# Optimization experiments

Hardware: AMD Instinct MI355X
Metric: run time of the kernel (lower is better)

## Reference

```python
import jax, jax.numpy as jnp
import numpy as np

B, N, C, H = 8, 1024, 512, 8
DH = C // H
SCALE = DH ** -0.5
NEG = -1.0e9


def setup_inputs() -> dict:
    key = jax.random.key(0)
    ks = jax.random.split(key, 8)
    s = lambda fan: 1.0 / np.sqrt(fan)
    return {
        "x": jax.random.normal(ks[0], (B, N, C), jnp.float32),
        "mask": jnp.ones((B, N), jnp.float32),
        "qkv_w": jax.random.normal(ks[1], (3 * C, C), jnp.float32) * s(C),
        "qkv_b": jnp.zeros((3 * C,), jnp.float32),
        "proj_w_mat": jax.random.normal(ks[2], (C, C), jnp.float32) * s(C),
        "proj_b": jnp.zeros((C,), jnp.float32),
        "pl_w": jax.random.normal(ks[3], (H, H), jnp.float32) * s(H),
        "pl_b": jnp.zeros((H,), jnp.float32),
        "pw_w": jax.random.normal(ks[4], (H, H), jnp.float32) * s(H),
        "pw_b": jnp.zeros((H,), jnp.float32),
    }


def reference(x, mask, qkv_w, qkv_b, proj_w_mat, proj_b, pl_w, pl_b, pw_w, pw_b):
    b, n, c = x.shape
    h = pl_w.shape[0]
    dh = c // h
    # qkv: [B,N,3C] -> [3,B,H,N,Dh]
    qkv = (x @ qkv_w.T + qkv_b).reshape(b, n, 3, h, dh).transpose(2, 0, 3, 1, 4)
    q, k, v = qkv[0] * SCALE, qkv[1], qkv[2]
    # raw scores [B,H,N,N]
    attn = jnp.einsum("bhnd,bhmd->bhnm", q, k)
    # talking-heads pre-softmax mixing (Linear over head dim)
    attn = jnp.einsum("bhnm,gh->bgnm", attn, pl_w) + pl_b[None, :, None, None]
    # mask: [B,N] -> broadcast over heads and query dim (keys masked)
    attn = attn + (1.0 - mask)[:, None, None, :] * NEG
    attn = jax.nn.softmax(attn, axis=-1)
    # talking-heads post-softmax mixing
    attn = jnp.einsum("bhnm,gh->bgnm", attn, pw_w) + pw_b[None, :, None, None]
    out = jnp.einsum("bhnm,bhmd->bhnd", attn, v)
    out = out.transpose(0, 2, 1, 3).reshape(b, n, c)
    out = out @ proj_w_mat.T + proj_b
    return (out, attn)
```

## Files before the change

kernel.cpp:

```cpp
#include <hip/hip_runtime.h>
#include <cstddef>

#define B_ 8
#define N_ 1024
#define C_ 512
#define H_ 8
#define DH_ 64
#define QKVLD 1536
#define SCALE_ 0.125f
#define NEG_ -1.0e9f

typedef _Float16 f16;
typedef f16  f16x4 __attribute__((ext_vector_type(4)));
typedef f16  f16x8 __attribute__((ext_vector_type(8)));
typedef float f32x4 __attribute__((ext_vector_type(4)));

static __device__ __forceinline__ f16x4 cvt4(float4 v) {
    f16x4 r; r[0] = (f16)v.x; r[1] = (f16)v.y; r[2] = (f16)v.z; r[3] = (f16)v.w;
    return r;
}

template<int BN, bool BHALF>
__device__ __forceinline__ void gemm_core(
    const float* __restrict__ A, int lda,
    const void* __restrict__ Bv, int ldb,
    const float* __restrict__ bias, float scale,
    float* __restrict__ Cc, int ldc, int K, int bm, int bn)
{
    constexpr int FJ = BN / 32;
    __shared__ __align__(16) f16 Af[128][40];
    __shared__ __align__(16) f16 Bf[BN][40];
    const int tid  = threadIdx.x;
    const int wid  = tid >> 6, lane = tid & 63;
    const int wm   = (wid >> 1) * 64, wn = (wid & 1) * (BN / 2);
    const int lrow = lane & 15, kg = lane >> 4;
    const int ar = tid >> 3, ac = (tid & 7) << 2;
    const int hr = tid >> 2, hc = (tid & 3) << 3;

    f32x4 acc[4][FJ];
#pragma unroll
    for (int i = 0; i < 4; ++i)
#pragma unroll
        for (int j = 0; j < FJ; ++j) acc[i][j] = (f32x4){0.f, 0.f, 0.f, 0.f};

    for (int k0 = 0; k0 < K; k0 += 32) {
        float4 a0 = *(const float4*)(A + (size_t)(bm + ar     ) * lda + k0 + ac);
        float4 a1 = *(const float4*)(A + (size_t)(bm + ar + 32) * lda + k0 + ac);
        float4 a2 = *(const float4*)(A + (size_t)(bm + ar + 64) * lda + k0 + ac);
        float4 a3 = *(const float4*)(A + (size_t)(bm + ar + 96) * lda + k0 + ac);
        float4 b0, b1, b2, b3;
        f16x8  bh;
        if constexpr (!BHALF) {
            const float* Bp = (const float*)Bv;
            b0 = *(const float4*)(Bp + (size_t)(bn + ar     ) * ldb + k0 + ac);
            b1 = *(const float4*)(Bp + (size_t)(bn + ar + 32) * ldb + k0 + ac);
            if constexpr (BN == 128) {
                b2 = *(const float4*)(Bp + (size_t)(bn + ar + 64) * ldb + k0 + ac);
                b3 = *(const float4*)(Bp + (size_t)(bn + ar + 96) * ldb + k0 + ac);
            }
        } else {
            const f16* Bp = (const f16*)Bv;
            bh = *(const f16x8*)(Bp + (size_t)(bn + hr) * ldb + k0 + hc);
        }
        __syncthreads();
        *(f16x4*)&Af[ar     ][ac] = cvt4(a0);
        *(f16x4*)&Af[ar + 32][ac] = cvt4(a1);
        *(f16x4*)&Af[ar + 64][ac] = cvt4(a2);
        *(f16x4*)&Af[ar + 96][ac] = cvt4(a3);
        if constexpr (!BHALF) {
            *(f16x4*)&Bf[ar     ][ac] = cvt4(b0);
            *(f16x4*)&Bf[ar + 32][ac] = cvt4(b1);
            if constexpr (BN == 128) {
                *(f16x4*)&Bf[ar + 64][ac] = cvt4(b2);
                *(f16x4*)&Bf[ar + 96][ac] = cvt4(b3);
            }
        } else {
            *(f16x8*)&Bf[hr][hc] = bh;
        }
        __syncthreads();
        f16x8 af[4], bf[FJ];
#pragma unroll
        for (int i = 0; i < 4; ++i)
            af[i] = *(const f16x8*)&Af[wm + i * 16 + lrow][kg * 8];
#pragma unroll
        for (int j = 0; j < FJ; ++j)
            bf[j] = *(const f16x8*)&Bf[wn + j * 16 + lrow][kg * 8];
#pragma unroll
        for (int i = 0; i < 4; ++i)
#pragma unroll
            for (int j = 0; j < FJ; ++j)
                acc[i][j] = __builtin_amdgcn_mfma_f32_16x16x32_f16(af[i], bf[j], acc[i][j], 0, 0, 0);
    }
#pragma unroll
    for (int j = 0; j < FJ; ++j) {
        const int col = bn + wn + j * 16 + lrow;
        const float bv = bias ? bias[col] : 0.f;
#pragma unroll
        for (int i = 0; i < 4; ++i) {
            const int row0 = bm + wm + i * 16 + kg * 4;
#pragma unroll
            for (int r = 0; r < 4; ++r)
                Cc[(size_t)(row0 + r) * ldc + col] = acc[i][j][r] * scale + bv;
        }
    }
}

__global__ __launch_bounds__(256) void k_qkv(const float* __restrict__ x,
                                             const float* __restrict__ w,
                                             const float* __restrict__ b,
                                             float* __restrict__ o) {
    gemm_core<128, false>(x, C_, w, C_, b, 1.f, o, QKVLD, C_,
                          blockIdx.y * 128, blockIdx.x * 128);
}

__global__ __launch_bounds__(256) void k_proj(const float* __restrict__ o1,
                                              const float* __restrict__ w,
                                              const float* __restrict__ b,
                                              float* __restrict__ o) {
    gemm_core<128, false>(o1, C_, w, C_, b, 1.f, o, C_, C_,
                          blockIdx.y * 128, blockIdx.x * 128);
}

__global__ __launch_bounds__(256) void k_scores(const float* __restrict__ qkv,
                                                float* __restrict__ attn) {
    const int z = blockIdx.z, b = z >> 3, h = z & 7;
    const float* Q  = qkv + (size_t)b * N_ * QKVLD + h * DH_;
    const float* Kp = Q + C_;
    gemm_core<128, false>(Q, QKVLD, Kp, QKVLD, nullptr, SCALE_,
                          attn + (size_t)z * N_ * N_, N_, DH_,
                          blockIdx.y * 128, blockIdx.x * 128);
}

__global__ __launch_bounds__(256) void k_pv(const float* __restrict__ attn,
                                            const f16* __restrict__ vt,
                                            float* __restrict__ out1) {
    const int z = blockIdx.z, b = z >> 3, h = z & 7;
    gemm_core<64, true>(attn + (size_t)z * N_ * N_, N_,
                        vt + (size_t)z * DH_ * N_, N_, nullptr, 1.f,
                        out1 + (size_t)b * N_ * C_ + h * DH_, C_, N_,
                        blockIdx.y * 128, 0);
}

__global__ __launch_bounds__(256) void pack_vt(const float* __restrict__ qkv,
                                               f16* __restrict__ vt) {
    const int z = blockIdx.x, b = z >> 3, h = z & 7;
    const float* V = qkv + (size_t)b * N_ * QKVLD + 2 * C_ + h * DH_;
    f16* O = vt + (size_t)z * DH_ * N_;
    __shared__ __align__(16) f16 T[64][72];
    const int t = threadIdx.x;
    for (int m0 = 0; m0 < N_; m0 += 64) {
#pragma unroll
        for (int it = 0; it < 4; ++it) {
            const int m = (t >> 4) + it * 16, dg = t & 15, d = dg * 4;
            float4 v = *(const float4*)(V + (size_t)(m0 + m) * QKVLD + d);
            T[d + 0][m] = (f16)v.x; T[d + 1][m] = (f16)v.y;
            T[d + 2][m] = (f16)v.z; T[d + 3][m] = (f16)v.w;
        }
        __syncthreads();
#pragma unroll
        for (int it = 0; it < 2; ++it) {
            const int d = (t >> 3) + it * 32, m = (t & 7) << 3;
            *(f16x8*)(O + (size_t)d * N_ + m0 + m) = *(const f16x8*)&T[d][m];
        }
        __syncthreads();
    }
}

__global__ __launch_bounds__(256) void mix_softmax_kernel(
    float* __restrict__ attn, const float* __restrict__ mask,
    const float* __restrict__ pl_w, const float* __restrict__ pl_b,
    const float* __restrict__ pw_w, const float* __restrict__ pw_b)
{
    const int n = blockIdx.x;
    const int b = blockIdx.y;
    const int tid = threadIdx.x;
    __shared__ float w1[64], w2[64], b1[8], b2[8];
    __shared__ float red[4][8];
    if (tid < 64) w1[tid] = pl_w[tid];
    else if (tid < 128) w2[tid - 64] = pw_w[tid - 64];
    else if (tid < 136) b1[tid - 128] = pl_b[tid - 128];
    else if (tid < 144) b2[tid - 136] = pw_b[tid - 136];
    __syncthreads();

    const int m0 = tid << 2;
    const size_t rowbase = ((size_t)(b * H_) * N_ + n) * N_ + m0;
    const size_t hstride = (size_t)N_ * N_;

    float s[8][4];
#pragma unroll
    for (int h = 0; h < 8; ++h) {
        float4 v = *(const float4*)(attn + rowbase + (size_t)h * hstride);
        s[h][0] = v.x; s[h][1] = v.y; s[h][2] = v.z; s[h][3] = v.w;
    }
    float4 mv = *(const float4*)(mask + b * N_ + m0);
    const float mk[4] = {(1.f - mv.x) * NEG_, (1.f - mv.y) * NEG_,
                         (1.f - mv.z) * NEG_, (1.f - mv.w) * NEG_};
    float a[8][4];
#pragma unroll
    for (int g = 0; g < 8; ++g)
#pragma unroll
        for (int j = 0; j < 4; ++j) a[g][j] = b1[g] + mk[j];
#pragma unroll
    for (int h = 0; h < 8; ++h)
#pragma unroll
        for (int g = 0; g < 8; ++g) {
            const float w = w1[g * 8 + h];
#pragma unroll
            for (int j = 0; j < 4; ++j) a[g][j] = fmaf(w, s[h][j], a[g][j]);
        }
    float mx[8];
#pragma unroll
    for (int g = 0; g < 8; ++g)
        mx[g] = fmaxf(fmaxf(a[g][0], a[g][1]), fmaxf(a[g][2], a[g][3]));
#pragma unroll
    for (int g = 0; g < 8; ++g)
        for (int off = 32; off; off >>= 1)
            mx[g] = fmaxf(mx[g], __shfl_xor(mx[g], off));
    const int wv = tid >> 6, ln = tid & 63;
    if (ln == 0) {
#pragma unroll
        for (int g = 0; g < 8; ++g) red[wv][g] = mx[g];
    }
    __syncthreads();
#pragma unroll
    for (int g = 0; g < 8; ++g)
        mx[g] = fmaxf(fmaxf(red[0][g], red[1][g]), fmaxf(red[2][g], red[3][g]));
    __syncthreads();
    float sm[8];
#pragma unroll
    for (int g = 0; g < 8; ++g) {
        float t = 0.f;
#pragma unroll
        for (int j = 0; j < 4; ++j) {
            a[g][j] = __expf(a[g][j] - mx[g]);
            t += a[g][j];
        }
        sm[g] = t;
    }
#pragma unroll
    for (int g = 0; g < 8; ++g)
        for (int off = 32; off; off >>= 1)
            sm[g] += __shfl_xor(sm[g], off);
    if (ln == 0) {
#pragma unroll
        for (int g = 0; g < 8; ++g) red[wv][g] = sm[g];
    }
    __syncthreads();
#pragma unroll
    for (int g = 0; g < 8; ++g) {
        const float inv = 1.f / (red[0][g] + red[1][g] + red[2][g] + red[3][g]);
#pragma unroll
        for (int j = 0; j < 4; ++j) a[g][j] *= inv;
    }
#pragma unroll
    for (int g = 0; g < 8; ++g) {
        float o[4] = {b2[g], b2[g], b2[g], b2[g]};
#pragma unroll
        for (int h = 0; h < 8; ++h) {
            const float w = w2[g * 8 + h];
#pragma unroll
            for (int j = 0; j < 4; ++j) o[j] = fmaf(w, a[h][j], o[j]);
        }
        *(float4*)(attn + rowbase + (size_t)g * hstride) = make_float4(o[0], o[1], o[2], o[3]);
    }
}

extern "C" void kernel_launch(void* const* d_in, const int* in_sizes, int n_in,
                              void* d_out, int out_size, void* d_ws, size_t ws_size,
                              hipStream_t stream)
{
    const float* x      = (const float*)d_in[0];
    const float* mask   = (const float*)d_in[1];
    const float* qkv_w  = (const float*)d_in[2];
    const float* qkv_b  = (const float*)d_in[3];
    const float* proj_w = (const float*)d_in[4];
    const float* proj_b = (const float*)d_in[5];
    const float* pl_w   = (const float*)d_in[6];
    const float* pl_b   = (const float*)d_in[7];
    const float* pw_w   = (const float*)d_in[8];
    const float* pw_b   = (const float*)d_in[9];

    float* out  = (float*)d_out;
    float* attn = out + (size_t)B_ * N_ * C_;
    float* qkv  = (float*)d_ws;
    float* out1 = qkv + (size_t)B_ * N_ * 3 * C_;
    f16*   vt   = (f16*)(out1 + (size_t)B_ * N_ * C_);
    (void)in_sizes; (void)n_in; (void)out_size; (void)ws_size;

    k_qkv<<<dim3(QKVLD / 128, B_ * N_ / 128), 256, 0, stream>>>(x, qkv_w, qkv_b, qkv);

    pack_vt<<<dim3(B_ * H_), 256, 0, stream>>>(qkv, vt);

    k_scores<<<dim3(N_ / 128, N_ / 128, B_ * H_), 256, 0, stream>>>(qkv, attn);

    mix_softmax_kernel<<<dim3(N_, B_), 256, 0, stream>>>(attn, mask, pl_w, pl_b, pw_w, pw_b);

    k_pv<<<dim3(1, N_ / 128, B_ * H_), 256, 0, stream>>>(attn, vt, out1);

    k_proj<<<dim3(C_ / 128, B_ * N_ / 128), 256, 0, stream>>>(out1, proj_w, proj_b, out);
}
```

Baseline: 318.2 us.

## Fuse scores, talking-heads softmax, PV and projection into one flash-style kernel

Replaces the separate score GEMM, mix/softmax pass, PV GEMM and projection GEMM with one kernel per 32-query tile. It runs two passes over the keys: the first recomputes scores with online max/sum statistics, the second recomputes them to write the normalized mixed attention, accumulate PV, and then apply the output projection. K and proj_w are pre-packed to fp16. This removes the fp32 attention round-trip read/write between kernels but doubles the QK compute. The grid is also small (256 blocks) with per-lane global K loads, which may limit occupancy and bandwidth.

```diff
diff --git a/kernel.cpp b/kernel.cpp
--- a/kernel.cpp
+++ b/kernel.cpp
@@ -35,7 +35,6 @@
     const int wm   = (wid >> 1) * 64, wn = (wid & 1) * (BN / 2);
     const int lrow = lane & 15, kg = lane >> 4;
     const int ar = tid >> 3, ac = (tid & 7) << 2;
-    const int hr = tid >> 2, hc = (tid & 3) << 3;
 
     f32x4 acc[4][FJ];
 #pragma unroll
@@ -48,48 +47,33 @@
         float4 a1 = *(const float4*)(A + (size_t)(bm + ar + 32) * lda + k0 + ac);
         float4 a2 = *(const float4*)(A + (size_t)(bm + ar + 64) * lda + k0 + ac);
         float4 a3 = *(const float4*)(A + (size_t)(bm + ar + 96) * lda + k0 + ac);
-        float4 b0, b1, b2, b3;
-        f16x8  bh;
-        if constexpr (!BHALF) {
-            const float* Bp = (const float*)Bv;
-            b0 = *(const float4*)(Bp + (size_t)(bn + ar     ) * ldb + k0 + ac);
-            b1 = *(const float4*)(Bp + (size_t)(bn + ar + 32) * ldb + k0 + ac);
-            if constexpr (BN == 128) {
-                b2 = *(const float4*)(Bp + (size_t)(bn + ar + 64) * ldb + k0 + ac);
-                b3 = *(const float4*)(Bp + (size_t)(bn + ar + 96) * ldb + k0 + ac);
-            }
-        } else {
-            const f16* Bp = (const f16*)Bv;
-            bh = *(const f16x8*)(Bp + (size_t)(bn + hr) * ldb + k0 + hc);
-        }
+        const float* Bp = (const float*)Bv;
+        float4 b0 = *(const float4*)(Bp + (size_t)(bn + ar     ) * ldb + k0 + ac);
+        float4 b1 = *(const float4*)(Bp + (size_t)(bn + ar + 32) * ldb + k0 + ac);
+        float4 b2 = *(const float4*)(Bp + (size_t)(bn + ar + 64) * ldb + k0 + ac);
+        float4 b3 = *(const float4*)(Bp + (size_t)(bn + ar + 96) * ldb + k0 + ac);
         __syncthreads();
         *(f16x4*)&Af[ar     ][ac] = cvt4(a0);
         *(f16x4*)&Af[ar + 32][ac] = cvt4(a1);
         *(f16x4*)&Af[ar + 64][ac] = cvt4(a2);
         *(f16x4*)&Af[ar + 96][ac] = cvt4(a3);
-        if constexpr (!BHALF) {
-            *(f16x4*)&Bf[ar     ][ac] = cvt4(b0);
-            *(f16x4*)&Bf[ar + 32][ac] = cvt4(b1);
-            if constexpr (BN == 128) {
-                *(f16x4*)&Bf[ar + 64][ac] = cvt4(b2);
-                *(f16x4*)&Bf[ar + 96][ac] = cvt4(b3);
-            }
-        } else {
-            *(f16x8*)&Bf[hr][hc] = bh;
-        }
-        __syncthreads();
-        f16x8 af[4], bf[FJ];
+        *(f16x4*)&Bf[ar     ][ac] = cvt4(b0);
+        *(f16x4*)&Bf[ar + 32][ac] = cvt4(b1);
+        *(f16x4*)&Bf[ar + 64][ac] = cvt4(b2);
+        *(f16x4*)&Bf[ar + 96][ac] = cvt4(b3);
+        __syncthreads();
+        f16x8 af[4], bfv[FJ];
 #pragma unroll
         for (int i = 0; i < 4; ++i)
             af[i] = *(const f16x8*)&Af[wm + i * 16 + lrow][kg * 8];
 #pragma unroll
         for (int j = 0; j < FJ; ++j)
-            bf[j] = *(const f16x8*)&Bf[wn + j * 16 + lrow][kg * 8];
+            bfv[j] = *(const f16x8*)&Bf[wn + j * 16 + lrow][kg * 8];
 #pragma unroll
         for (int i = 0; i < 4; ++i)
 #pragma unroll
             for (int j = 0; j < FJ; ++j)
-                acc[i][j] = __builtin_amdgcn_mfma_f32_16x16x32_f16(af[i], bf[j], acc[i][j], 0, 0, 0);
+                acc[i][j] = __builtin_amdgcn_mfma_f32_16x16x32_f16(af[i], bfv[j], acc[i][j], 0, 0, 0);
     }
 #pragma unroll
     for (int j = 0; j < FJ; ++j) {
@@ -113,32 +97,30 @@
                           blockIdx.y * 128, blockIdx.x * 128);
 }
 
-__global__ __launch_bounds__(256) void k_proj(const float* __restrict__ o1,
-                                              const float* __restrict__ w,
-                                              const float* __restrict__ b,
-                                              float* __restrict__ o) {
-    gemm_core<128, false>(o1, C_, w, C_, b, 1.f, o, C_, C_,
-                          blockIdx.y * 128, blockIdx.x * 128);
-}
-
-__global__ __launch_bounds__(256) void k_scores(const float* __restrict__ qkv,
-                                                float* __restrict__ attn) {
-    const int z = blockIdx.z, b = z >> 3, h = z & 7;
-    const float* Q  = qkv + (size_t)b * N_ * QKVLD + h * DH_;
-    const float* Kp = Q + C_;
-    gemm_core<128, false>(Q, QKVLD, Kp, QKVLD, nullptr, SCALE_,
-                          attn + (size_t)z * N_ * N_, N_, DH_,
-                          blockIdx.y * 128, blockIdx.x * 128);
-}
-
-__global__ __launch_bounds__(256) void k_pv(const float* __restrict__ attn,
-                                            const f16* __restrict__ vt,
-                                            float* __restrict__ out1) {
-    const int z = blockIdx.z, b = z >> 3, h = z & 7;
-    gemm_core<64, true>(attn + (size_t)z * N_ * N_, N_,
-                        vt + (size_t)z * DH_ * N_, N_, nullptr, 1.f,
-                        out1 + (size_t)b * N_ * C_ + h * DH_, C_, N_,
-                        blockIdx.y * 128, 0);
+__global__ __launch_bounds__(256) void pack_kf(const float* __restrict__ qkv,
+                                               f16* __restrict__ kf) {
+    const size_t i8 = ((size_t)blockIdx.x * 256 + threadIdx.x) << 3;
+    const size_t row = i8 >> 9;
+    const int c = (int)(i8 & 511);
+    const float* src = qkv + row * QKVLD + C_ + c;
+    float4 v0 = *(const float4*)src;
+    float4 v1 = *(const float4*)(src + 4);
+    f16x8 o;
+    o[0]=(f16)v0.x; o[1]=(f16)v0.y; o[2]=(f16)v0.z; o[3]=(f16)v0.w;
+    o[4]=(f16)v1.x; o[5]=(f16)v1.y; o[6]=(f16)v1.z; o[7]=(f16)v1.w;
+    *(f16x8*)(kf + i8) = o;
+}
+
+__global__ __launch_bounds__(256) void pack_pw(const float* __restrict__ w,
+                                               f16* __restrict__ wf) {
+    const size_t i8 = ((size_t)blockIdx.x * 256 + threadIdx.x) << 3;
+    const float* src = w + i8;
+    float4 v0 = *(const float4*)src;
+    float4 v1 = *(const float4*)(src + 4);
+    f16x8 o;
+    o[0]=(f16)v0.x; o[1]=(f16)v0.y; o[2]=(f16)v0.z; o[3]=(f16)v0.w;
+    o[4]=(f16)v1.x; o[5]=(f16)v1.y; o[6]=(f16)v1.z; o[7]=(f16)v1.w;
+    *(f16x8*)(wf + i8) = o;
 }
 
 __global__ __launch_bounds__(256) void pack_vt(const float* __restrict__ qkv,
@@ -151,7 +133,7 @@
     for (int m0 = 0; m0 < N_; m0 += 64) {
 #pragma unroll
         for (int it = 0; it < 4; ++it) {
-            const int m = (t >> 4) + it * 16, dg = t & 15, d = dg * 4;
+            const int m = (t >> 4) + it * 16, d = (t & 15) * 4;
             float4 v = *(const float4*)(V + (size_t)(m0 + m) * QKVLD + d);
             T[d + 0][m] = (f16)v.x; T[d + 1][m] = (f16)v.y;
             T[d + 2][m] = (f16)v.z; T[d + 3][m] = (f16)v.w;
@@ -166,102 +148,253 @@
     }
 }
 
-__global__ __launch_bounds__(256) void mix_softmax_kernel(
-    float* __restrict__ attn, const float* __restrict__ mask,
+__global__ __launch_bounds__(256, 2) void fused_attn(
+    const float* __restrict__ qkv,
+    const f16*  __restrict__ kf,
+    const f16*  __restrict__ vt,
+    const f16*  __restrict__ pwf,
+    const float* __restrict__ mask,
     const float* __restrict__ pl_w, const float* __restrict__ pl_b,
-    const float* __restrict__ pw_w, const float* __restrict__ pw_b)
+    const float* __restrict__ pw_w, const float* __restrict__ pw_b,
+    const float* __restrict__ proj_b,
+    float* __restrict__ attn,
+    float* __restrict__ out)
 {
-    const int n = blockIdx.x;
-    const int b = blockIdx.y;
+    __shared__ __align__(16) f16 Qs[32][520];
+    __shared__ __align__(16) f16 Ps[8][32][40];
+    __shared__ float Stat[2][2][8][2][16];
+
+    const int qt = blockIdx.x, b = blockIdx.y;
+    const int q0 = qt * 32;
     const int tid = threadIdx.x;
-    __shared__ float w1[64], w2[64], b1[8], b2[8];
-    __shared__ float red[4][8];
-    if (tid < 64) w1[tid] = pl_w[tid];
-    else if (tid < 128) w2[tid - 64] = pw_w[tid - 64];
-    else if (tid < 136) b1[tid - 128] = pl_b[tid - 128];
-    else if (tid < 144) b2[tid - 136] = pw_b[tid - 136];
+    const int w = tid >> 6, l = tid & 63;
+    const int wq = w >> 1, wm = w & 1;
+    const int qh = wq << 4, mh = wm << 4;
+    const int lc = l & 15, lr4 = l >> 4;
+
+    {
+        const int qrow = tid >> 3, c0 = (tid & 7) << 6;
+        const float* src = qkv + (size_t)(b * N_ + q0 + qrow) * QKVLD + c0;
+#pragma unroll
+        for (int c = 0; c < 64; c += 4) {
+            float4 v = *(const float4*)(src + c);
+            f16x4 o;
+            o[0]=(f16)(v.x*SCALE_); o[1]=(f16)(v.y*SCALE_);
+            o[2]=(f16)(v.z*SCALE_); o[3]=(f16)(v.w*SCALE_);
+            *(f16x4*)&Qs[qrow][c0 + c] = o;
+        }
+    }
     __syncthreads();
 
-    const int m0 = tid << 2;
-    const size_t rowbase = ((size_t)(b * H_) * N_ + n) * N_ + m0;
-    const size_t hstride = (size_t)N_ * N_;
-
-    float s[8][4];
-#pragma unroll
-    for (int h = 0; h < 8; ++h) {
-        float4 v = *(const float4*)(attn + rowbase + (size_t)h * hstride);
-        s[h][0] = v.x; s[h][1] = v.y; s[h][2] = v.z; s[h][3] = v.w;
-    }
-    float4 mv = *(const float4*)(mask + b * N_ + m0);
-    const float mk[4] = {(1.f - mv.x) * NEG_, (1.f - mv.y) * NEG_,
-                         (1.f - mv.z) * NEG_, (1.f - mv.w) * NEG_};
-    float a[8][4];
-#pragma unroll
-    for (int g = 0; g < 8; ++g)
-#pragma unroll
-        for (int j = 0; j < 4; ++j) a[g][j] = b1[g] + mk[j];
-#pragma unroll
-    for (int h = 0; h < 8; ++h)
+    const f16* kfb = kf + (size_t)b * N_ * C_;
+    const float* maskb = mask + b * N_;
+
+    float mx[8], sm[8];
+#pragma unroll
+    for (int g = 0; g < 8; ++g) { mx[g] = -3.0e38f; sm[g] = 0.f; }
+
+    for (int mt = 0; mt < N_; mt += 32) {
+        float4 mk4 = *(const float4*)(maskb + mt + mh + (lr4 << 2));
+        float mkv[4] = {(1.f-mk4.x)*NEG_, (1.f-mk4.y)*NEG_,
+                        (1.f-mk4.z)*NEG_, (1.f-mk4.w)*NEG_};
+        float a[8][4];
 #pragma unroll
         for (int g = 0; g < 8; ++g) {
-            const float w = w1[g * 8 + h];
-#pragma unroll
-            for (int j = 0; j < 4; ++j) a[g][j] = fmaf(w, s[h][j], a[g][j]);
-        }
-    float mx[8];
-#pragma unroll
-    for (int g = 0; g < 8; ++g)
-        mx[g] = fmaxf(fmaxf(a[g][0], a[g][1]), fmaxf(a[g][2], a[g][3]));
-#pragma unroll
-    for (int g = 0; g < 8; ++g)
-        for (int off = 32; off; off >>= 1)
-            mx[g] = fmaxf(mx[g], __shfl_xor(mx[g], off));
-    const int wv = tid >> 6, ln = tid & 63;
-    if (ln == 0) {
-#pragma unroll
-        for (int g = 0; g < 8; ++g) red[wv][g] = mx[g];
+            const float bb = pl_b[g];
+#pragma unroll
+            for (int r = 0; r < 4; ++r) a[g][r] = bb + mkv[r];
+        }
+#pragma unroll
+        for (int h = 0; h < 8; ++h) {
+            f32x4 s = (f32x4){0.f, 0.f, 0.f, 0.f};
+#pragma unroll
+            for (int kk = 0; kk < 2; ++kk) {
+                const int c = (h << 6) + (kk << 5) + (lr4 << 3);
+                f16x8 af = *(const f16x8*)(kfb + (size_t)(mt + mh + lc) * C_ + c);
+                f16x8 bf = *(const f16x8*)&Qs[qh + lc][c];
+                s = __builtin_amdgcn_mfma_f32_16x16x32_f16(af, bf, s, 0, 0, 0);
+            }
+#pragma unroll
+            for (int g = 0; g < 8; ++g) {
+                const float wv = pl_w[(g << 3) + h];
+#pragma unroll
+                for (int r = 0; r < 4; ++r) a[g][r] = fmaf(wv, s[r], a[g][r]);
+            }
+        }
+#pragma unroll
+        for (int g = 0; g < 8; ++g) {
+            float pm = fmaxf(fmaxf(a[g][0], a[g][1]), fmaxf(a[g][2], a[g][3]));
+            float nm = fmaxf(mx[g], pm);
+            float t  = sm[g] * __expf(mx[g] - nm);
+#pragma unroll
+            for (int r = 0; r < 4; ++r) t += __expf(a[g][r] - nm);
+            sm[g] = t; mx[g] = nm;
+        }
+    }
+#pragma unroll
+    for (int g = 0; g < 8; ++g) {
+#pragma unroll
+        for (int off = 16; off < 64; off <<= 1) {
+            float m2 = __shfl_xor(mx[g], off);
+            float s2 = __shfl_xor(sm[g], off);
+            float nm = fmaxf(mx[g], m2);
+            sm[g] = sm[g] * __expf(mx[g] - nm) + s2 * __expf(m2 - nm);
+            mx[g] = nm;
+        }
+    }
+    if (l < 16) {
+#pragma unroll
+        for (int g = 0; g < 8; ++g) {
+            Stat[wq][wm][g][0][l] = mx[g];
+            Stat[wq][wm][g][1][l] = sm[g];
+        }
     }
     __syncthreads();
-#pragma unroll
-    for (int g = 0; g < 8; ++g)
-        mx[g] = fmaxf(fmaxf(red[0][g], red[1][g]), fmaxf(red[2][g], red[3][g]));
+    float invs[8];
+#pragma unroll
+    for (int g = 0; g < 8; ++g) {
+        float m2 = Stat[wq][wm ^ 1][g][0][lc];
+        float s2 = Stat[wq][wm ^ 1][g][1][lc];
+        float nm = fmaxf(mx[g], m2);
+        sm[g] = sm[g] * __expf(mx[g] - nm) + s2 * __expf(m2 - nm);
+        mx[g] = nm;
+        invs[g] = 1.f / sm[g];
+    }
+
+    float* attnb = attn + (size_t)(b * H_) * N_ * N_;
+    f32x4 O[2][2][4];
+#pragma unroll
+    for (int gp = 0; gp < 2; ++gp)
+#pragma unroll
+        for (int qf = 0; qf < 2; ++qf)
+#pragma unroll
+            for (int df = 0; df < 4; ++df) O[gp][qf][df] = (f32x4){0.f,0.f,0.f,0.f};
+    const int gg0 = w << 1;
+
+    for (int mt = 0; mt < N_; mt += 32) {
+        float4 mk4 = *(const float4*)(maskb + mt + mh + (lr4 << 2));
+        float mkv[4] = {(1.f-mk4.x)*NEG_, (1.f-mk4.y)*NEG_,
+                        (1.f-mk4.z)*NEG_, (1.f-mk4.w)*NEG_};
+        float a[8][4];
+#pragma unroll
+        for (int g = 0; g < 8; ++g) {
+            const float bb = pl_b[g];
+#pragma unroll
+            for (int r = 0; r < 4; ++r) a[g][r] = bb + mkv[r];
+        }
+#pragma unroll
+        for (int h = 0; h < 8; ++h) {
+            f32x4 s = (f32x4){0.f, 0.f, 0.f, 0.f};
+#pragma unroll
+            for (int kk = 0; kk < 2; ++kk) {
+                const int c = (h << 6) + (kk << 5) + (lr4 << 3);
+                f16x8 af = *(const f16x8*)(kfb + (size_t)(mt + mh + lc) * C_ + c);
+                f16x8 bf = *(const f16x8*)&Qs[qh + lc][c];
+                s = __builtin_amdgcn_mfma_f32_16x16x32_f16(af, bf, s, 0, 0, 0);
+            }
+#pragma unroll
+            for (int g = 0; g < 8; ++g) {
+                const float wv = pl_w[(g << 3) + h];
+#pragma unroll
+                for (int r = 0; r < 4; ++r) a[g][r] = fmaf(wv, s[r], a[g][r]);
+            }
+        }
+        float p[8][4];
+#pragma unroll
+        for (int g = 0; g < 8; ++g)
+#pragma unroll
+            for (int r = 0; r < 4; ++r)
+                p[g][r] = __expf(a[g][r] - mx[g]) * invs[g];
+
+        const int qg = q0 + qh + lc;
+        const int mg = mt + mh + (lr4 << 2);
+#pragma unroll
+        for (int gg = 0; gg < 8; ++gg) {
+            const float bb = pw_b[gg];
+            float o0 = bb, o1 = bb, o2 = bb, o3 = bb;
+#pragma unroll
+            for (int g = 0; g < 8; ++g) {
+                const float wv = pw_w[(gg << 3) + g];
+                o0 = fmaf(wv, p[g][0], o0);
+                o1 = fmaf(wv, p[g][1], o1);
+                o2 = fmaf(wv, p[g][2], o2);
+                o3 = fmaf(wv, p[g][3], o3);
+            }
+            *(float4*)(attnb + ((size_t)gg * N_ + qg) * N_ + mg) =
+                make_float4(o0, o1, o2, o3);
+            f16x4 ph; ph[0]=(f16)o0; ph[1]=(f16)o1; ph[2]=(f16)o2; ph[3]=(f16)o3;
+            *(f16x4*)&Ps[gg][qh + lc][mh + (lr4 << 2)] = ph;
+        }
+        __syncthreads();
+#pragma unroll
+        for (int gp = 0; gp < 2; ++gp) {
+            const int gg = gg0 + gp;
+            const f16* vg = vt + ((size_t)(b * H_ + gg)) * DH_ * N_ + mt + (lr4 << 3);
+            f16x8 afr[4];
+#pragma unroll
+            for (int df = 0; df < 4; ++df)
+                afr[df] = *(const f16x8*)(vg + (size_t)((df << 4) + lc) * N_);
+#pragma unroll
+            for (int qf = 0; qf < 2; ++qf) {
+                f16x8 bfr = *(const f16x8*)&Ps[gg][(qf << 4) + lc][lr4 << 3];
+#pragma unroll
+                for (int df = 0; df < 4; ++df)
+                    O[gp][qf][df] = __builtin_amdgcn_mfma_f32_16x16x32_f16(
+                        afr[df], bfr, O[gp][qf][df], 0, 0, 0);
+            }
+        }
+        __syncthreads();
+    }
+
+#pragma unroll
+    for (int gp = 0; gp < 2; ++gp)
+#pragma unroll
+        for (int qf = 0; qf < 2; ++qf)
+#pragma unroll
+            for (int df = 0; df < 4; ++df) {
+                f16x4 ph;
+                ph[0]=(f16)O[gp][qf][df][0]; ph[1]=(f16)O[gp][qf][df][1];
+                ph[2]=(f16)O[gp][qf][df][2]; ph[3]=(f16)O[gp][qf][df][3];
+                *(f16x4*)&Qs[(qf << 4) + lc][((gg0 + gp) << 6) + (df << 4) + (lr4 << 2)] = ph;
+            }
     __syncthreads();
-    float sm[8];
-#pragma unroll
-    for (int g = 0; g < 8; ++g) {
-        float t = 0.f;
-#pragma unroll
-        for (int j = 0; j < 4; ++j) {
-            a[g][j] = __expf(a[g][j] - mx[g]);
-            t += a[g][j];
-        }
-        sm[g] = t;
-    }
-#pragma unroll
-    for (int g = 0; g < 8; ++g)
-        for (int off = 32; off; off >>= 1)
-            sm[g] += __shfl_xor(sm[g], off);
-    if (ln == 0) {
-#pragma unroll
-        for (int g = 0; g < 8; ++g) red[wv][g] = sm[g];
-    }
-    __syncthreads();
-#pragma unroll
-    for (int g = 0; g < 8; ++g) {
-        const float inv = 1.f / (red[0][g] + red[1][g] + red[2][g] + red[3][g]);
-#pragma unroll
-        for (int j = 0; j < 4; ++j) a[g][j] *= inv;
-    }
-#pragma unroll
-    for (int g = 0; g < 8; ++g) {
-        float o[4] = {b2[g], b2[g], b2[g], b2[g]};
-#pragma unroll
-        for (int h = 0; h < 8; ++h) {
-            const float w = w2[g * 8 + h];
-#pragma unroll
-            for (int j = 0; j < 4; ++j) o[j] = fmaf(w, a[h][j], o[j]);
-        }
-        *(float4*)(attn + rowbase + (size_t)g * hstride) = make_float4(o[0], o[1], o[2], o[3]);
+
+    {
+        f32x4 acc[8][2];
+#pragma unroll
+        for (int cof = 0; cof < 8; ++cof)
+#pragma unroll
+            for (int qf = 0; qf < 2; ++qf) acc[cof][qf] = (f32x4){0.f,0.f,0.f,0.f};
+        const int co_w = w << 7;
+        for (int ci = 0; ci < C_; ci += 32) {
+            f16x8 bfr[2];
+#pragma unroll
+            for (int qf = 0; qf < 2; ++qf)
+                bfr[qf] = *(const f16x8*)&Qs[(qf << 4) + lc][ci + (lr4 << 3)];
+#pragma unroll
+            for (int cof = 0; cof < 8; ++cof) {
+                f16x8 afr = *(const f16x8*)(pwf + (size_t)(co_w + (cof << 4) + lc) * C_ + ci + (lr4 << 3));
+#pragma unroll
+                for (int qf = 0; qf < 2; ++qf)
+                    acc[cof][qf] = __builtin_amdgcn_mfma_f32_16x16x32_f16(
+                        afr, bfr[qf], acc[cof][qf], 0, 0, 0);
+            }
+        }
+        float* outb = out + (size_t)(b * N_ + q0) * C_;
+#pragma unroll
+        for (int cof = 0; cof < 8; ++cof) {
+            const int co = co_w + (cof << 4) + (lr4 << 2);
+            float4 bias4 = *(const float4*)(proj_b + co);
+#pragma unroll
+            for (int qf = 0; qf < 2; ++qf) {
+                float4 r;
+                r.x = acc[cof][qf][0] + bias4.x;
+                r.y = acc[cof][qf][1] + bias4.y;
+                r.z = acc[cof][qf][2] + bias4.z;
+                r.w = acc[cof][qf][3] + bias4.w;
+                *(float4*)(outb + (size_t)((qf << 4) + lc) * C_ + co) = r;
+            }
+        }
     }
 }
 
@@ -282,20 +415,18 @@
 
     float* out  = (float*)d_out;
     float* attn = out + (size_t)B_ * N_ * C_;
-    float* qkv  = (float*)d_ws;
-    float* out1 = qkv + (size_t)B_ * N_ * 3 * C_;
-    f16*   vt   = (f16*)(out1 + (size_t)B_ * N_ * C_);
+    float* qkvb = (float*)d_ws;
+    f16*   kf   = (f16*)(qkvb + (size_t)B_ * N_ * 3 * C_);
+    f16*   vt   = kf + (size_t)B_ * N_ * C_;
+    f16*   pwf  = vt + (size_t)B_ * N_ * C_;
     (void)in_sizes; (void)n_in; (void)out_size; (void)ws_size;
 
-    k_qkv<<<dim3(QKVLD / 128, B_ * N_ / 128), 256, 0, stream>>>(x, qkv_w, qkv_b, qkv);
-
-    pack_vt<<<dim3(B_ * H_), 256, 0, stream>>>(qkv, vt);
-
-    k_scores<<<dim3(N_ / 128, N_ / 128, B_ * H_), 256, 0, stream>>>(qkv, attn);
-
-    mix_softmax_kernel<<<dim3(N_, B_), 256, 0, stream>>>(attn, mask, pl_w, pl_b, pw_w, pw_b);
-
-    k_pv<<<dim3(1, N_ / 128, B_ * H_), 256, 0, stream>>>(attn, vt, out1);
-
-    k_proj<<<dim3(C_ / 128, B_ * N_ / 128), 256, 0, stream>>>(out1, proj_w, proj_b, out);
-}
+    k_qkv<<<dim3(QKVLD / 128, B_ * N_ / 128), 256, 0, stream>>>(x, qkv_w, qkv_b, qkvb);
+
+    pack_kf<<<dim3(2048), 256, 0, stream>>>(qkvb, kf);
+    pack_vt<<<dim3(B_ * H_), 256, 0, stream>>>(qkvb, vt);
+    pack_pw<<<dim3(128), 256, 0, stream>>>(proj_w, pwf);
+
+    fused_attn<<<dim3(N_ / 32, B_), 256, 0, stream>>>(
+        qkvb, kf, vt, pwf, mask, pl_w, pl_b, pw_w, pw_b, proj_b, attn, out);
+}
```

After: 364.0 us. +14.4%, slower.
